# Performance work log

Hardware: AMD Instinct MI355X
Metric: run time of the kernel (lower is better)

The kernel has to match this reference:

```python
import jax, jax.numpy as jnp
import numpy as np

HEADS = 16

def setup_inputs() -> dict:
    key = jax.random.key(0)
    k1, k2, k3, k4 = jax.random.split(key, 4)
    B, T, S, W = 2, 2048, 2048, 1024
    x = jax.random.normal(k1, (B, T, W), dtype=jnp.float32)
    cond_k = jax.random.normal(k2, (B, S, W), dtype=jnp.float32)
    cond_v = jax.random.normal(k3, (B, S, W), dtype=jnp.float32)
    w_proj = jax.random.normal(k4, (W, W), dtype=jnp.float32) * 0.02
    b_proj = jnp.zeros((W,), dtype=jnp.float32)
    return {"x": x, "cond_k": cond_k, "cond_v": cond_v, "w_proj": w_proj, "b_proj": b_proj}

def reference(x, cond_k, cond_v, w_proj, b_proj):
    B, T, W = x.shape
    S = cond_k.shape[1]
    H = HEADS
    d = W // H
    scale = 1.0 / jnp.sqrt(jnp.sqrt(jnp.float32(d)))  # applied to both q and k
    q = x.reshape(B, T, H, d) * scale
    k = cond_k.reshape(B, S, H, d) * scale
    v = cond_v.reshape(B, S, H, d)
    # scores: [B, H, T, S]
    scores = jnp.einsum('bthd,bshd->bhts', q, k)
    w = jax.nn.softmax(scores.astype(jnp.float32), axis=-1).astype(scores.dtype)
    out = jnp.einsum('bhts,bshd->bthd', w, v).reshape(B, T, W)
    # c_proj: torch Linear -> x @ W.T + b
    return out @ w_proj.T + b_proj
```

## Files before the change

### kernel.cpp

```cpp
#include <hip/hip_runtime.h>

#define Bn 2
#define Hn 16
#define Tn 2048
#define Sn 2048
#define Wd 1024
#define Dh 64

typedef __attribute__((ext_vector_type(8))) short s16x8;
typedef __attribute__((ext_vector_type(4))) short s16x4;
typedef __attribute__((ext_vector_type(4))) float f32x4;
typedef __attribute__((ext_vector_type(2))) unsigned u32x2;

#define MFMA(a, b, c) __builtin_amdgcn_mfma_f32_16x16x32_bf16((a), (b), (c), 0, 0, 0)

__device__ __forceinline__ s16x8 ld8(const short* p) { return *(const s16x8*)p; }

__device__ __forceinline__ short f2bf(float f) {
    unsigned u = __builtin_bit_cast(unsigned, f);
    u += 0x7FFFu + ((u >> 16) & 1u);
    return (short)(u >> 16);
}

__global__ void cvt_scale(const float* __restrict__ in, short* __restrict__ out,
                          int n, float s) {
    int i = (blockIdx.x * 256 + threadIdx.x) * 8;
    if (i < n) {
        float4 a = *(const float4*)(in + i);
        float4 b = *(const float4*)(in + i + 4);
        s16x8 o;
        o[0] = f2bf(a.x * s); o[1] = f2bf(a.y * s); o[2] = f2bf(a.z * s); o[3] = f2bf(a.w * s);
        o[4] = f2bf(b.x * s); o[5] = f2bf(b.y * s); o[6] = f2bf(b.z * s); o[7] = f2bf(b.w * s);
        *(s16x8*)(out + i) = o;
    }
}

__global__ __launch_bounds__(256) void vtrans(const float* __restrict__ cv,
                                              short* __restrict__ vt) {
    __shared__ short T[64][68];
    const int st = blockIdx.x & 31;
    const int bh = blockIdx.x >> 5;
    const int b = bh >> 4, h = bh & 15;
    const int tid = threadIdx.x;
#pragma unroll
    for (int i = 0; i < 4; ++i) {
        int f = i * 256 + tid, sr = f >> 4, c4 = f & 15;
        float4 v = *(const float4*)(cv + (size_t)(b * Sn + st * 64 + sr) * Wd + h * Dh + c4 * 4);
        s16x4 o;
        o[0] = f2bf(v.x); o[1] = f2bf(v.y); o[2] = f2bf(v.z); o[3] = f2bf(v.w);
        *(s16x4*)&T[sr][c4 * 4] = o;
    }
    __syncthreads();
#pragma unroll
    for (int i = 0; i < 4; ++i) {
        int f = i * 256 + tid, dr = f >> 4, p4 = f & 15;
        s16x4 o;
#pragma unroll
        for (int k = 0; k < 4; ++k) {
            o[k] = T[k * 16 + p4][dr];
        }
        *(s16x4*)(vt + (size_t)(bh * Dh + dr) * Sn + st * 64 + p4 * 4) = o;
    }
}

#define KSTR 72

__global__ __launch_bounds__(256, 2) void attn_fused(
    const float* __restrict__ x, const short* __restrict__ kb,
    const short* __restrict__ vt, short* __restrict__ ao)
{
    __shared__ alignas(16) short Ks[2][64 * KSTR];
    __shared__ alignas(16) short Vs[2][64 * KSTR];
    __shared__ alignas(16) short Pt[4][32 * KSTR];

    const int tid  = threadIdx.x;
    const int w    = tid >> 6;
    const int l    = tid & 63;
    const int quad = l >> 4;
    const int l16  = l & 15;

    const int bh = blockIdx.x & 31;
    const int qt = blockIdx.x >> 5;
    const int b  = bh >> 4, h = bh & 15;

    const int qrow0 = qt * 128 + w * 32;

    const float SQ = 0.125f * 1.4426950408889634f;
    s16x8 aq[2][2];
#pragma unroll
    for (int mi = 0; mi < 2; ++mi)
#pragma unroll
        for (int c = 0; c < 2; ++c) {
            const float* p = x + (size_t)(b * Tn + qrow0 + mi * 16 + l16) * Wd
                               + h * Dh + c * 32 + quad * 8;
            float4 a = ((const float4*)p)[0], bb = ((const float4*)p)[1];
            s16x8 o;
            o[0] = f2bf(a.x * SQ); o[1] = f2bf(a.y * SQ); o[2] = f2bf(a.z * SQ); o[3] = f2bf(a.w * SQ);
            o[4] = f2bf(bb.x * SQ); o[5] = f2bf(bb.y * SQ); o[6] = f2bf(bb.z * SQ); o[7] = f2bf(bb.w * SQ);
            aq[mi][c] = o;
        }

    f32x4 oacc[2][4];
    float dn[2][4];
#pragma unroll
    for (int mi = 0; mi < 2; ++mi) {
#pragma unroll
        for (int nt = 0; nt < 4; ++nt) {
            oacc[mi][nt][0] = 0.f; oacc[mi][nt][1] = 0.f;
            oacc[mi][nt][2] = 0.f; oacc[mi][nt][3] = 0.f;
        }
#pragma unroll
        for (int r = 0; r < 4; ++r) dn[mi][r] = 0.f;
    }

    const short* kb_h = kb + (size_t)(b * Sn) * Wd + h * Dh;
    const short* vt_h = vt + (size_t)(bh * Dh) * Sn;

    const int sr = tid >> 3;
    const int sg = tid & 7;

    short* Pw = &Pt[w][0];

    s16x8 kr[2], vr[2];
#pragma unroll
    for (int i = 0; i < 2; ++i) {
        int r0 = sr + i * 32;
        kr[i] = ld8(kb_h + (size_t)r0 * Wd + sg * 8);
        vr[i] = ld8(vt_h + (size_t)r0 * Sn + sg * 8);
    }
#pragma unroll
    for (int i = 0; i < 2; ++i) {
        int r0 = sr + i * 32;
        *(s16x8*)&Ks[0][r0 * KSTR + sg * 8] = kr[i];
        *(s16x8*)&Vs[0][r0 * KSTR + sg * 8] = vr[i];
    }
    __syncthreads();

    const int NIT = Sn / 64;
    for (int it = 0; it < NIT; ++it) {
        const int p = it & 1;

        if (it + 1 < NIT) {
            const int s1 = (it + 1) * 64;
#pragma unroll
            for (int i = 0; i < 2; ++i) {
                int r0 = sr + i * 32;
                kr[i] = ld8(kb_h + (size_t)(s1 + r0) * Wd + sg * 8);
                vr[i] = ld8(vt_h + (size_t)r0 * Sn + s1 + sg * 8);
            }
        }

        f32x4 sc[2][4];
        const f32x4 z = {0.f, 0.f, 0.f, 0.f};
        __builtin_amdgcn_s_setprio(1);
#pragma unroll
        for (int sj = 0; sj < 4; ++sj) {
            s16x8 k0 = *(const s16x8*)&Ks[p][(sj * 16 + l16) * KSTR + quad * 8];
            s16x8 k1 = *(const s16x8*)&Ks[p][(sj * 16 + l16) * KSTR + 32 + quad * 8];
#pragma unroll
            for (int mi = 0; mi < 2; ++mi) {
                sc[mi][sj] = MFMA(aq[mi][0], k0, z);
                sc[mi][sj] = MFMA(aq[mi][1], k1, sc[mi][sj]);
            }
        }
        __builtin_amdgcn_s_setprio(0);

#pragma unroll
        for (int mi = 0; mi < 2; ++mi)
#pragma unroll
            for (int r = 0; r < 4; ++r) {
                unsigned u0 = __builtin_bit_cast(unsigned, __builtin_amdgcn_exp2f(sc[mi][0][r]));
                unsigned u1 = __builtin_bit_cast(unsigned, __builtin_amdgcn_exp2f(sc[mi][1][r]));
                unsigned u2 = __builtin_bit_cast(unsigned, __builtin_amdgcn_exp2f(sc[mi][2][r]));
                unsigned u3 = __builtin_bit_cast(unsigned, __builtin_amdgcn_exp2f(sc[mi][3][r]));
                unsigned h1 = u1 & 0xFFFF0000u;
                unsigned h3 = u3 & 0xFFFF0000u;
                unsigned w0 = (u0 >> 16) | h1;
                unsigned w1 = (u2 >> 16) | h3;
                float t0 = __builtin_bit_cast(float, u0 & 0xFFFF0000u)
                         + __builtin_bit_cast(float, h1);
                float t1 = __builtin_bit_cast(float, u2 & 0xFFFF0000u)
                         + __builtin_bit_cast(float, h3);
                dn[mi][r] += t0 + t1;
                u32x2 pk; pk[0] = w0; pk[1] = w1;
                *(u32x2*)&Pw[(mi * 16 + quad * 4 + r) * KSTR + l16 * 4] = pk;
            }
        __asm__ __volatile__("" ::: "memory");

        s16x8 ap[2][2], bv[4][2];
#pragma unroll
        for (int mi = 0; mi < 2; ++mi)
#pragma unroll
            for (int g = 0; g < 2; ++g)
                ap[mi][g] = *(const s16x8*)&Pw[(mi * 16 + l16) * KSTR + g * 32 + quad * 8];
#pragma unroll
        for (int nt = 0; nt < 4; ++nt)
#pragma unroll
            for (int g = 0; g < 2; ++g)
                bv[nt][g] = *(const s16x8*)&Vs[p][(nt * 16 + l16) * KSTR + g * 32 + quad * 8];
        __builtin_amdgcn_s_setprio(1);
#pragma unroll
        for (int mi = 0; mi < 2; ++mi)
#pragma unroll
            for (int nt = 0; nt < 4; ++nt) {
                oacc[mi][nt] = MFMA(ap[mi][0], bv[nt][0], oacc[mi][nt]);
                oacc[mi][nt] = MFMA(ap[mi][1], bv[nt][1], oacc[mi][nt]);
            }
        __builtin_amdgcn_s_setprio(0);

        if (it + 1 < NIT) {
#pragma unroll
            for (int i = 0; i < 2; ++i) {
                int r0 = sr + i * 32;
                *(s16x8*)&Ks[p ^ 1][r0 * KSTR + sg * 8] = kr[i];
                *(s16x8*)&Vs[p ^ 1][r0 * KSTR + sg * 8] = vr[i];
            }
        }
        __syncthreads();
    }

#pragma unroll
    for (int mi = 0; mi < 2; ++mi)
#pragma unroll
        for (int r = 0; r < 4; ++r) {
            float d = dn[mi][r];
            d += __shfl_xor(d, 1);
            d += __shfl_xor(d, 2);
            d += __shfl_xor(d, 4);
            d += __shfl_xor(d, 8);
            float inv = 1.0f / d;
            int t = qrow0 + mi * 16 + quad * 4 + r;
#pragma unroll
            for (int nt = 0; nt < 4; ++nt)
                ao[(size_t)(b * Tn + t) * Wd + h * Dh + nt * 16 + l16] =
                    f2bf(oacc[mi][nt][r] * inv);
        }
}

#define LSTR 40

__global__ __launch_bounds__(256, 2) void proj_gemm(
    const short* __restrict__ A, const short* __restrict__ Wb,
    const float* __restrict__ bias, float* __restrict__ out)
{
    __shared__ alignas(16) short As[2][128 * LSTR];
    __shared__ alignas(16) short Bs[2][64 * LSTR];

    const int tid  = threadIdx.x;
    const int w    = tid >> 6;
    const int l    = tid & 63;
    const int quad = l >> 4;
    const int l16  = l & 15;

    const int bn = blockIdx.x & 15;
    const int bm = blockIdx.x >> 4;
    const int m0 = bm * 128;
    const int n0 = bn * 64;
    const int wm = (w & 1) * 64;
    const int wn = (w >> 1) * 32;

    const int rr = tid >> 2;
    const int sg = tid & 3;

    f32x4 acc[4][2];
#pragma unroll
    for (int mi = 0; mi < 4; ++mi)
#pragma unroll
        for (int nt = 0; nt < 2; ++nt) {
            acc[mi][nt][0] = 0.f; acc[mi][nt][1] = 0.f;
            acc[mi][nt][2] = 0.f; acc[mi][nt][3] = 0.f;
        }

    s16x8 ra0 = ld8(A  + (size_t)(m0 + rr) * Wd + sg * 8);
    s16x8 ra1 = ld8(A  + (size_t)(m0 + 64 + rr) * Wd + sg * 8);
    s16x8 rb  = ld8(Wb + (size_t)(n0 + rr) * Wd + sg * 8);
    *(s16x8*)&As[0][rr * LSTR + sg * 8]        = ra0;
    *(s16x8*)&As[0][(rr + 64) * LSTR + sg * 8] = ra1;
    *(s16x8*)&Bs[0][rr * LSTR + sg * 8]        = rb;
    __syncthreads();

    for (int k0 = 0; k0 < Wd; k0 += 32) {
        const int p = (k0 >> 5) & 1;

        if (k0 + 32 < Wd) {
            ra0 = ld8(A  + (size_t)(m0 + rr) * Wd + k0 + 32 + sg * 8);
            ra1 = ld8(A  + (size_t)(m0 + 64 + rr) * Wd + k0 + 32 + sg * 8);
            rb  = ld8(Wb + (size_t)(n0 + rr) * Wd + k0 + 32 + sg * 8);
        }

        s16x8 a[4], bw[2];
#pragma unroll
        for (int mi = 0; mi < 4; ++mi)
            a[mi] = *(const s16x8*)&As[p][(wm + mi * 16 + l16) * LSTR + quad * 8];
#pragma unroll
        for (int nt = 0; nt < 2; ++nt)
            bw[nt] = *(const s16x8*)&Bs[p][(wn + nt * 16 + l16) * LSTR + quad * 8];
        __builtin_amdgcn_s_setprio(1);
#pragma unroll
        for (int mi = 0; mi < 4; ++mi)
#pragma unroll
            for (int nt = 0; nt < 2; ++nt)
                acc[mi][nt] = MFMA(a[mi], bw[nt], acc[mi][nt]);
        __builtin_amdgcn_s_setprio(0);

        if (k0 + 32 < Wd) {
            *(s16x8*)&As[p ^ 1][rr * LSTR + sg * 8]        = ra0;
            *(s16x8*)&As[p ^ 1][(rr + 64) * LSTR + sg * 8] = ra1;
            *(s16x8*)&Bs[p ^ 1][rr * LSTR + sg * 8]        = rb;
        }
        __syncthreads();
    }

#pragma unroll
    for (int nt = 0; nt < 2; ++nt) {
        float bv = bias[n0 + wn + nt * 16 + l16];
#pragma unroll
        for (int mi = 0; mi < 4; ++mi)
#pragma unroll
            for (int r = 0; r < 4; ++r)
                out[(size_t)(m0 + wm + mi * 16 + quad * 4 + r) * Wd + n0 + wn + nt * 16 + l16] =
                    acc[mi][nt][r] + bv;
    }
}

extern "C" void kernel_launch(void* const* d_in, const int* in_sizes, int n_in,
                              void* d_out, int out_size, void* d_ws, size_t ws_size,
                              hipStream_t stream) {
    const float* x  = (const float*)d_in[0];
    const float* ck = (const float*)d_in[1];
    const float* cv = (const float*)d_in[2];
    const float* wp = (const float*)d_in[3];
    const float* bp = (const float*)d_in[4];

    const int nX = Bn * Tn * Wd;
    const int nW = Wd * Wd;

    short* kbb = (short*)d_ws;
    short* vtb = kbb + nX;
    short* wbb = vtb + nX;
    short* am  = wbb + nW;

    cvt_scale<<<dim3(nX / 2048), dim3(256), 0, stream>>>(ck, kbb, nX, 1.0f);
    cvt_scale<<<dim3(nW / 2048), dim3(256), 0, stream>>>(wp, wbb, nW, 1.0f);
    vtrans<<<dim3(1024), dim3(256), 0, stream>>>(cv, vtb);

    attn_fused<<<dim3(Bn * Hn * (Tn / 128)), dim3(256), 0, stream>>>(x, kbb, vtb, am);
    proj_gemm<<<dim3((Bn * Tn / 128) * (Wd / 64)), dim3(256), 0, stream>>>(
        am, wbb, bp, (float*)d_out);
}
```

Baseline: 168.4 us.

## Keep softmax probabilities in registers by transposing the QK MFMA and permuting V

Swaps the MFMA operand order so the score tile comes out transposed, letting each lane pack its exp values straight into the A operand of the PV MFMA without going through LDS. The V transpose kernel permutes S positions to match the new register layout, the per-wave P scratch buffer is removed, and bf16 packing uses the hardware v_cvt_pk_bf16_f32 instruction. The denominator is now summed over the unrounded fp32 exps rather than the bf16-truncated ones, and the row sum is reduced across quads and broadcast with a shuffle. This removes the LDS round trip and the extra synchronization cost for P, at the price of a more intricate index permutation that must match exactly.

```diff
diff --git a/kernel.cpp b/kernel.cpp
--- a/kernel.cpp
+++ b/kernel.cpp
@@ -10,7 +10,7 @@
 typedef __attribute__((ext_vector_type(8))) short s16x8;
 typedef __attribute__((ext_vector_type(4))) short s16x4;
 typedef __attribute__((ext_vector_type(4))) float f32x4;
-typedef __attribute__((ext_vector_type(2))) unsigned u32x2;
+typedef __attribute__((ext_vector_type(4))) unsigned u32x4;
 
 #define MFMA(a, b, c) __builtin_amdgcn_mfma_f32_16x16x32_bf16((a), (b), (c), 0, 0, 0)
 
@@ -20,6 +20,12 @@
     unsigned u = __builtin_bit_cast(unsigned, f);
     u += 0x7FFFu + ((u >> 16) & 1u);
     return (short)(u >> 16);
+}
+
+__device__ __forceinline__ unsigned cvtpk(float lo, float hi) {
+    unsigned r;
+    asm("v_cvt_pk_bf16_f32 %0, %1, %2" : "=v"(r) : "v"(lo), "v"(hi));
+    return r;
 }
 
 __global__ void cvt_scale(const float* __restrict__ in, short* __restrict__ out,
@@ -57,7 +63,8 @@
         s16x4 o;
 #pragma unroll
         for (int k = 0; k < 4; ++k) {
-            o[k] = T[k * 16 + p4][dr];
+            int sl = ((p4 >> 3) * 2 + (p4 & 1)) * 16 + ((p4 >> 1) & 3) * 4 + k;
+            o[k] = T[sl][dr];
         }
         *(s16x4*)(vt + (size_t)(bh * Dh + dr) * Sn + st * 64 + p4 * 4) = o;
     }
@@ -71,7 +78,6 @@
 {
     __shared__ alignas(16) short Ks[2][64 * KSTR];
     __shared__ alignas(16) short Vs[2][64 * KSTR];
-    __shared__ alignas(16) short Pt[4][32 * KSTR];
 
     const int tid  = threadIdx.x;
     const int w    = tid >> 6;
@@ -101,7 +107,7 @@
         }
 
     f32x4 oacc[2][4];
-    float dn[2][4];
+    float dn[2];
 #pragma unroll
     for (int mi = 0; mi < 2; ++mi) {
 #pragma unroll
@@ -109,8 +115,7 @@
             oacc[mi][nt][0] = 0.f; oacc[mi][nt][1] = 0.f;
             oacc[mi][nt][2] = 0.f; oacc[mi][nt][3] = 0.f;
         }
-#pragma unroll
-        for (int r = 0; r < 4; ++r) dn[mi][r] = 0.f;
+        dn[mi] = 0.f;
     }
 
     const short* kb_h = kb + (size_t)(b * Sn) * Wd + h * Dh;
@@ -118,8 +123,6 @@
 
     const int sr = tid >> 3;
     const int sg = tid & 7;
-
-    short* Pw = &Pt[w][0];
 
     s16x8 kr[2], vr[2];
 #pragma unroll
@@ -159,40 +162,37 @@
             s16x8 k1 = *(const s16x8*)&Ks[p][(sj * 16 + l16) * KSTR + 32 + quad * 8];
 #pragma unroll
             for (int mi = 0; mi < 2; ++mi) {
-                sc[mi][sj] = MFMA(aq[mi][0], k0, z);
-                sc[mi][sj] = MFMA(aq[mi][1], k1, sc[mi][sj]);
+                sc[mi][sj] = MFMA(k0, aq[mi][0], z);
+                sc[mi][sj] = MFMA(k1, aq[mi][1], sc[mi][sj]);
             }
         }
         __builtin_amdgcn_s_setprio(0);
 
-#pragma unroll
-        for (int mi = 0; mi < 2; ++mi)
-#pragma unroll
-            for (int r = 0; r < 4; ++r) {
-                unsigned u0 = __builtin_bit_cast(unsigned, __builtin_amdgcn_exp2f(sc[mi][0][r]));
-                unsigned u1 = __builtin_bit_cast(unsigned, __builtin_amdgcn_exp2f(sc[mi][1][r]));
-                unsigned u2 = __builtin_bit_cast(unsigned, __builtin_amdgcn_exp2f(sc[mi][2][r]));
-                unsigned u3 = __builtin_bit_cast(unsigned, __builtin_amdgcn_exp2f(sc[mi][3][r]));
-                unsigned h1 = u1 & 0xFFFF0000u;
-                unsigned h3 = u3 & 0xFFFF0000u;
-                unsigned w0 = (u0 >> 16) | h1;
-                unsigned w1 = (u2 >> 16) | h3;
-                float t0 = __builtin_bit_cast(float, u0 & 0xFFFF0000u)
-                         + __builtin_bit_cast(float, h1);
-                float t1 = __builtin_bit_cast(float, u2 & 0xFFFF0000u)
-                         + __builtin_bit_cast(float, h3);
-                dn[mi][r] += t0 + t1;
-                u32x2 pk; pk[0] = w0; pk[1] = w1;
-                *(u32x2*)&Pw[(mi * 16 + quad * 4 + r) * KSTR + l16 * 4] = pk;
-            }
-        __asm__ __volatile__("" ::: "memory");
-
-        s16x8 ap[2][2], bv[4][2];
-#pragma unroll
-        for (int mi = 0; mi < 2; ++mi)
-#pragma unroll
-            for (int g = 0; g < 2; ++g)
-                ap[mi][g] = *(const s16x8*)&Pw[(mi * 16 + l16) * KSTR + g * 32 + quad * 8];
+        s16x8 ap[2][2];
+#pragma unroll
+        for (int mi = 0; mi < 2; ++mi) {
+            float ex[4][4];
+#pragma unroll
+            for (int sj = 0; sj < 4; ++sj)
+#pragma unroll
+                for (int r = 0; r < 4; ++r)
+                    ex[sj][r] = __builtin_amdgcn_exp2f(sc[mi][sj][r]);
+            dn[mi] += (((ex[0][0] + ex[0][1]) + (ex[0][2] + ex[0][3]))
+                     + ((ex[1][0] + ex[1][1]) + (ex[1][2] + ex[1][3])))
+                    + (((ex[2][0] + ex[2][1]) + (ex[2][2] + ex[2][3]))
+                     + ((ex[3][0] + ex[3][1]) + (ex[3][2] + ex[3][3])));
+#pragma unroll
+            for (int g = 0; g < 2; ++g) {
+                u32x4 pk;
+                pk[0] = cvtpk(ex[2 * g][0],     ex[2 * g][1]);
+                pk[1] = cvtpk(ex[2 * g][2],     ex[2 * g][3]);
+                pk[2] = cvtpk(ex[2 * g + 1][0], ex[2 * g + 1][1]);
+                pk[3] = cvtpk(ex[2 * g + 1][2], ex[2 * g + 1][3]);
+                ap[mi][g] = __builtin_bit_cast(s16x8, pk);
+            }
+        }
+
+        s16x8 bv[4][2];
 #pragma unroll
         for (int nt = 0; nt < 4; ++nt)
 #pragma unroll
@@ -220,21 +220,21 @@
     }
 
 #pragma unroll
-    for (int mi = 0; mi < 2; ++mi)
+    for (int mi = 0; mi < 2; ++mi) {
+        float d = dn[mi];
+        d += __shfl_xor(d, 16);
+        d += __shfl_xor(d, 32);
+        float invl = 1.0f / d;
 #pragma unroll
         for (int r = 0; r < 4; ++r) {
-            float d = dn[mi][r];
-            d += __shfl_xor(d, 1);
-            d += __shfl_xor(d, 2);
-            d += __shfl_xor(d, 4);
-            d += __shfl_xor(d, 8);
-            float inv = 1.0f / d;
+            float inv = __shfl(invl, quad * 4 + r);
             int t = qrow0 + mi * 16 + quad * 4 + r;
 #pragma unroll
             for (int nt = 0; nt < 4; ++nt)
                 ao[(size_t)(b * Tn + t) * Wd + h * Dh + nt * 16 + l16] =
                     f2bf(oacc[mi][nt][r] * inv);
         }
+    }
 }
 
 #define LSTR 40
```

Measured after the change: 160.4 us. 4.7% less time.
